# Performance work log

Hardware: AMD Instinct MI355X
Metric: run time of the kernel (lower is better)

The kernel has to match this reference:

```python
import jax, jax.numpy as jnp
import numpy as np

K_CONST = 2.0
KERNEL = 5
ALPHA = 1e-4
BETA = 0.75


def setup_inputs() -> dict:
    key = jax.random.key(0)
    x = jax.random.normal(key, (16, 96, 224, 224), dtype=jnp.float32)
    return {"x": x}


def reference(x) -> jnp.ndarray:
    # Original: y = conv2d(x^2, ones(C,C,5,5), pad=2); out = x / (k + alpha*y)**beta.
    # The all-ones C x C filter sums x^2 over ALL channels and a 5x5 window,
    # producing an identical map for every output channel. Compute that sum
    # once on a single-channel tensor and broadcast -- same math, O(C) cheaper.
    s = jnp.sum(x * x, axis=1, keepdims=True)  # [B,1,H,W] channel-summed squares
    w = jnp.ones((1, 1, KERNEL, KERNEL), dtype=x.dtype)
    y = jax.lax.conv_general_dilated(
        s, w, window_strides=(1, 1), padding="SAME",
        dimension_numbers=("NCHW", "OIHW", "NCHW"),
    )  # [B,1,H,W], broadcasts against [B,C,H,W]
    return x / (K_CONST + ALPHA * y) ** BETA
```

## Files before the change

### kernel.cpp

```cpp
#include <hip/hip_runtime.h>
#include <math.h>


#define BB 16
#define CC 96
#define HH 224
#define WW 224
#define HW (HH * WW)
#define CHW (CC * HW)
#define NPIX (BB * HW)
#define W4 (WW / 4)
#define NCOL (BB * HH * W4)
#define CG 4
#define CPG (CC / CG)
#define S4 (HW / 4)

typedef float v4f __attribute__((ext_vector_type(4)));

__global__ __launch_bounds__(256) void lrn_sqsum(const float* __restrict__ x,
                                                 float* __restrict__ part) {
    int t  = blockIdx.x * 256 + threadIdx.x;
    int cg = blockIdx.y;
    int w4 = t % W4;
    int bh = t / W4;
    int b  = bh / HH;
    int h  = bh % HH;
    size_t idx = (((size_t)b * CHW + (size_t)h * WW) >> 2) + w4
               + (size_t)cg * CPG * S4;
    const v4f* xp = (const v4f*)x + idx;
    v4f acc = (v4f)(0.f);
    for (int c0 = 0; c0 < CPG; c0 += 8) {
        v4f v[8];
#pragma unroll
        for (int u = 0; u < 8; ++u) v[u] = xp[(size_t)(c0 + u) * S4];
#pragma unroll
        for (int u = 0; u < 8; ++u) acc += v[u] * v[u];
    }
    ((v4f*)part)[(size_t)cg * NCOL + t] = acc;
}

__global__ __launch_bounds__(256) void lrn_sum4(const float* __restrict__ part,
                                                float* __restrict__ s) {
    int t = blockIdx.x * 256 + threadIdx.x;
    const v4f* p = (const v4f*)part;
    v4f a = p[t];
    v4f b = p[(size_t)NCOL + t];
    v4f c = p[(size_t)2 * NCOL + t];
    v4f d = p[(size_t)3 * NCOL + t];
    ((v4f*)s)[t] = (a + b) + (c + d);
}

__global__ __launch_bounds__(256) void lrn_scale(const float* __restrict__ s,
                                                 float* __restrict__ sc) {
    int t = blockIdx.x * 256 + threadIdx.x;
    int w  = t % WW;
    int bh = t / WW;
    int h  = bh % HH;
    float y = 0.f;
#pragma unroll
    for (int dh = -2; dh <= 2; ++dh) {
        int hh = h + dh;
        if (hh < 0 || hh >= HH) continue;
        const float* row = s + (size_t)(bh + dh) * WW;
#pragma unroll
        for (int dw = -2; dw <= 2; ++dw) {
            int ww = w + dw;
            if (ww >= 0 && ww < WW) y += row[ww];
        }
    }
    sc[t] = powf(2.0f + 1e-4f * y, -0.75f);
}

__global__ __launch_bounds__(256) void lrn_norm(const float* __restrict__ x,
                                                const float* __restrict__ sc,
                                                float* __restrict__ out) {
    int t  = blockIdx.x * 256 + threadIdx.x;
    int cg = blockIdx.y;
    int w4 = t % W4;
    int bh = t / W4;
    int b  = bh / HH;
    int h  = bh % HH;
    v4f scv = ((const v4f*)sc)[t];
    size_t idx = (((size_t)b * CHW + (size_t)h * WW) >> 2) + w4
               + (size_t)cg * CPG * S4;
    const v4f* xp = (const v4f*)x + idx;
    v4f* op = (v4f*)out + idx;
    for (int c0 = 0; c0 < CPG; c0 += 8) {
        v4f v[8];
#pragma unroll
        for (int u = 0; u < 8; ++u) v[u] = xp[(size_t)(c0 + u) * S4];
#pragma unroll
        for (int u = 0; u < 8; ++u) op[(size_t)(c0 + u) * S4] = v[u] * scv;
    }
}

extern "C" void kernel_launch(void* const* d_in, const int* in_sizes, int n_in,
                              void* d_out, int out_size, void* d_ws, size_t ws_size,
                              hipStream_t stream) {
    const float* x = (const float*)d_in[0];
    float* out  = (float*)d_out;
    float* part = (float*)d_ws;
    float* s    = part + (size_t)CG * NPIX;
    float* sc   = s + NPIX;

    lrn_sqsum<<<dim3(NCOL / 256, CG), 256, 0, stream>>>(x, part);
    lrn_sum4 <<<NCOL / 256, 256, 0, stream>>>(part, s);
    lrn_scale<<<NPIX / 256, 256, 0, stream>>>(s, sc);
    lrn_norm <<<dim3(NCOL / 256, CG), 256, 0, stream>>>(x, sc, out);
}
```

Baseline: 580.9 us.

## Fuse LRN stages into one persistent kernel with grid barriers

Replaces four separate launches with a single persistent kernel that computes channel sums, the 5x5 window scale, and the normalization in phases separated by a software grid barrier. The partial-sum buffer and reduction pass are removed, and the final pass walks chunks in reverse order so recently read input may still be cached. Output writes use nontemporal stores. This risks lower memory-level parallelism from a fixed 512-block grid, load imbalance across chunks, and relies on all blocks being co-resident for the spin barrier.

```diff
diff --git a/kernel.cpp b/kernel.cpp
--- a/kernel.cpp
+++ b/kernel.cpp
@@ -11,86 +11,95 @@
 #define NPIX (BB * HW)
 #define W4 (WW / 4)
 #define NCOL (BB * HH * W4)
-#define CG 4
-#define CPG (CC / CG)
+#define NCHUNK (NCOL / 256)
 #define S4 (HW / 4)
+#define NBLK 512
+#define NTHR 256
+#define TTOT (NBLK * NTHR)
 
 typedef float v4f __attribute__((ext_vector_type(4)));
 
-__global__ __launch_bounds__(256) void lrn_sqsum(const float* __restrict__ x,
-                                                 float* __restrict__ part) {
-    int t  = blockIdx.x * 256 + threadIdx.x;
-    int cg = blockIdx.y;
-    int w4 = t % W4;
-    int bh = t / W4;
-    int b  = bh / HH;
-    int h  = bh % HH;
-    size_t idx = (((size_t)b * CHW + (size_t)h * WW) >> 2) + w4
-               + (size_t)cg * CPG * S4;
-    const v4f* xp = (const v4f*)x + idx;
-    v4f acc = (v4f)(0.f);
-    for (int c0 = 0; c0 < CPG; c0 += 8) {
-        v4f v[8];
-#pragma unroll
-        for (int u = 0; u < 8; ++u) v[u] = xp[(size_t)(c0 + u) * S4];
-#pragma unroll
-        for (int u = 0; u < 8; ++u) acc += v[u] * v[u];
+__device__ __forceinline__ void gbar(unsigned* cnt) {
+    __syncthreads();
+    if (threadIdx.x == 0) {
+        __threadfence();
+        atomicAdd(cnt, 1u);
+        while (__hip_atomic_load(cnt, __ATOMIC_RELAXED,
+                                 __HIP_MEMORY_SCOPE_AGENT) < (unsigned)NBLK)
+            __builtin_amdgcn_s_sleep(8);
+        __threadfence();
     }
-    ((v4f*)part)[(size_t)cg * NCOL + t] = acc;
+    __syncthreads();
 }
 
-__global__ __launch_bounds__(256) void lrn_sum4(const float* __restrict__ part,
-                                                float* __restrict__ s) {
-    int t = blockIdx.x * 256 + threadIdx.x;
-    const v4f* p = (const v4f*)part;
-    v4f a = p[t];
-    v4f b = p[(size_t)NCOL + t];
-    v4f c = p[(size_t)2 * NCOL + t];
-    v4f d = p[(size_t)3 * NCOL + t];
-    ((v4f*)s)[t] = (a + b) + (c + d);
-}
+__global__ void lrn_init(unsigned* bar) { bar[0] = 0u; bar[1] = 0u; }
 
-__global__ __launch_bounds__(256) void lrn_scale(const float* __restrict__ s,
-                                                 float* __restrict__ sc) {
-    int t = blockIdx.x * 256 + threadIdx.x;
-    int w  = t % WW;
-    int bh = t / WW;
-    int h  = bh % HH;
-    float y = 0.f;
+__global__ __launch_bounds__(NTHR, 2) void lrn_fused(
+        const float* __restrict__ x, float* __restrict__ out,
+        float* __restrict__ s, float* __restrict__ sc, unsigned* bar) {
+    const int tid = threadIdx.x;
+
+    for (int k = blockIdx.x; k < NCHUNK; k += NBLK) {
+        int t  = k * NTHR + tid;
+        int w4 = t % W4;
+        int bh = t / W4;
+        int b  = bh / HH;
+        int h  = bh % HH;
+        size_t base = (((size_t)b * CHW + (size_t)h * WW) >> 2) + w4;
+        const v4f* xp = (const v4f*)x + base;
+        v4f acc = (v4f)(0.f);
+        for (int c0 = 0; c0 < CC; c0 += 8) {
+            v4f v[8];
 #pragma unroll
-    for (int dh = -2; dh <= 2; ++dh) {
-        int hh = h + dh;
-        if (hh < 0 || hh >= HH) continue;
-        const float* row = s + (size_t)(bh + dh) * WW;
+            for (int u = 0; u < 8; ++u) v[u] = xp[(size_t)(c0 + u) * S4];
 #pragma unroll
-        for (int dw = -2; dw <= 2; ++dw) {
-            int ww = w + dw;
-            if (ww >= 0 && ww < WW) y += row[ww];
+            for (int u = 0; u < 8; ++u) acc += v[u] * v[u];
         }
+        ((v4f*)s)[t] = acc;
     }
-    sc[t] = powf(2.0f + 1e-4f * y, -0.75f);
-}
 
-__global__ __launch_bounds__(256) void lrn_norm(const float* __restrict__ x,
-                                                const float* __restrict__ sc,
-                                                float* __restrict__ out) {
-    int t  = blockIdx.x * 256 + threadIdx.x;
-    int cg = blockIdx.y;
-    int w4 = t % W4;
-    int bh = t / W4;
-    int b  = bh / HH;
-    int h  = bh % HH;
-    v4f scv = ((const v4f*)sc)[t];
-    size_t idx = (((size_t)b * CHW + (size_t)h * WW) >> 2) + w4
-               + (size_t)cg * CPG * S4;
-    const v4f* xp = (const v4f*)x + idx;
-    v4f* op = (v4f*)out + idx;
-    for (int c0 = 0; c0 < CPG; c0 += 8) {
-        v4f v[8];
+    gbar(&bar[0]);
+
+    for (int t = blockIdx.x * NTHR + tid; t < NPIX; t += TTOT) {
+        int w  = t % WW;
+        int bh = t / WW;
+        int h  = bh % HH;
+        float y = 0.f;
 #pragma unroll
-        for (int u = 0; u < 8; ++u) v[u] = xp[(size_t)(c0 + u) * S4];
+        for (int dh = -2; dh <= 2; ++dh) {
+            int hh = h + dh;
+            if (hh < 0 || hh >= HH) continue;
+            const float* row = s + (size_t)(bh + dh) * WW;
 #pragma unroll
-        for (int u = 0; u < 8; ++u) op[(size_t)(c0 + u) * S4] = v[u] * scv;
+            for (int dw = -2; dw <= 2; ++dw) {
+                int ww = w + dw;
+                if (ww >= 0 && ww < WW) y += row[ww];
+            }
+        }
+        sc[t] = powf(2.0f + 1e-4f * y, -0.75f);
+    }
+
+    gbar(&bar[1]);
+
+    for (int k = blockIdx.x; k < NCHUNK; k += NBLK) {
+        int rk = NCHUNK - 1 - k;
+        int t  = rk * NTHR + tid;
+        int w4 = t % W4;
+        int bh = t / W4;
+        int b  = bh / HH;
+        int h  = bh % HH;
+        size_t base = (((size_t)b * CHW + (size_t)h * WW) >> 2) + w4;
+        v4f scv = ((const v4f*)sc)[t];
+        const v4f* xp = (const v4f*)x + base;
+        v4f* op = (v4f*)out + base;
+        for (int c0 = 0; c0 < CC; c0 += 8) {
+            v4f v[8];
+#pragma unroll
+            for (int u = 0; u < 8; ++u) v[u] = xp[(size_t)(c0 + u) * S4];
+#pragma unroll
+            for (int u = 0; u < 8; ++u)
+                __builtin_nontemporal_store(v[u] * scv, &op[(size_t)(c0 + u) * S4]);
+        }
     }
 }
 
@@ -98,13 +107,11 @@
                               void* d_out, int out_size, void* d_ws, size_t ws_size,
                               hipStream_t stream) {
     const float* x = (const float*)d_in[0];
-    float* out  = (float*)d_out;
-    float* part = (float*)d_ws;
-    float* s    = part + (size_t)CG * NPIX;
-    float* sc   = s + NPIX;
+    float* out = (float*)d_out;
+    float* s   = (float*)d_ws;
+    float* sc  = s + NPIX;
+    unsigned* bar = (unsigned*)(sc + NPIX);
 
-    lrn_sqsum<<<dim3(NCOL / 256, CG), 256, 0, stream>>>(x, part);
-    lrn_sum4 <<<NCOL / 256, 256, 0, stream>>>(part, s);
-    lrn_scale<<<NPIX / 256, 256, 0, stream>>>(s, sc);
-    lrn_norm <<<dim3(NCOL / 256, CG), 256, 0, stream>>>(x, sc, out);
+    lrn_init<<<1, 1, 0, stream>>>(bar);
+    lrn_fused<<<NBLK, NTHR, 0, stream>>>(x, out, s, sc, bar);
 }
```

After: 686.9 us. +18.2%, slower.
